# Performance work log

Hardware: AMD Instinct MI355X
Metric: run time of the kernel (lower is better)

## Reference

```python
import jax, jax.numpy as jnp
import numpy as np

N = 50000          # nodes
E = 600000         # edges
D = 128            # g_dim = h1_dim = h2_dim
R = 8              # 2 * n_speakers**2, n_speakers=2
B = 10             # num_bases


def setup_inputs() -> dict:
    key = jax.random.key(0)
    ks = jax.random.split(key, 10)
    s = 1.0 / np.sqrt(D)
    return {
        "node_features": jax.random.normal(ks[0], (N, D), jnp.float32),
        "edge_index": jax.random.randint(ks[1], (2, E), 0, N, jnp.int64),
        "edge_type": jax.random.randint(ks[2], (E,), 0, R, jnp.int64),
        # RGCNConv params (basis decomposition)
        "basis": jax.random.normal(ks[3], (B, D, D), jnp.float32) * s,
        "comp": jax.random.normal(ks[4], (R, B), jnp.float32) * (1.0 / np.sqrt(B)),
        "root": jax.random.normal(ks[5], (D, D), jnp.float32) * s,
        "bias1": jnp.zeros((D,), jnp.float32),
        # GraphConv params
        "w_rel": jax.random.normal(ks[6], (D, D), jnp.float32) * s,
        "b_rel": jnp.zeros((D,), jnp.float32),
        "w_root": jax.random.normal(ks[7], (D, D), jnp.float32) * s,
    }


def reference(node_features, edge_index, edge_type, basis, comp, root, bias1, w_rel, b_rel, w_root):
    x = node_features
    n = x.shape[0]
    r = comp.shape[0]
    src, dst = edge_index[0], edge_index[1]

    # ---- RGCNConv (basis decomposition, per-relation mean aggregation) ----
    # project through bases once: [N, B, D]
    xb = jnp.einsum('ni,bio->nbo', x, basis)
    # per-edge message: combine bases with relation coefficients  [E, D]
    msg = jnp.einsum('eb,ebo->eo', comp[edge_type], xb[src])
    # per-(dst, relation) mean normalization
    seg = dst * r + edge_type                       # [E]
    cnt = jax.ops.segment_sum(jnp.ones((msg.shape[0],), x.dtype), seg, num_segments=n * r)
    norm = 1.0 / jnp.maximum(cnt[seg], 1.0)         # [E]
    agg = jax.ops.segment_sum(msg * norm[:, None], dst, num_segments=n)  # [N, D]
    h1 = agg + x @ root + bias1

    # ---- GraphConv (add aggregation of neighbors + root transform) ----
    nbr = jax.ops.segment_sum(h1[src], dst, num_segments=n)  # [N, D]
    out = nbr @ w_rel.T + b_rel + h1 @ w_root.T
    return out
```

## Files before the change

### kernel.cpp

```cpp
#include <hip/hip_runtime.h>
#include <stdint.h>

#define N_NODES 50000
#define E_EDGES 600000
#define D 128
#define R_REL 8
#define B_BASES 10
#define RN (R_REL * N_NODES)

typedef __attribute__((ext_vector_type(8))) short bf16x8;
typedef __attribute__((ext_vector_type(4))) float f32x4;

__device__ __forceinline__ short f2b(float f) {
    uint32_t u = __float_as_uint(f);
    u += 0x7fff + ((u >> 16) & 1);
    return (short)(u >> 16);
}
__device__ __forceinline__ float b2f(uint16_t u) {
    return __uint_as_float((uint32_t)u << 16);
}

__global__ __launch_bounds__(256) void k_front(const float* __restrict__ x,
                                               unsigned short* __restrict__ xb,
                                               const int* __restrict__ dst,
                                               const int* __restrict__ et,
                                               int* __restrict__ cntr,
                                               const float* __restrict__ basis,
                                               const float* __restrict__ comp,
                                               const float* __restrict__ root,
                                               const float* __restrict__ wrel,
                                               const float* __restrict__ wroot,
                                               short* __restrict__ wt,
                                               short* __restrict__ wrel_b,
                                               short* __restrict__ wroot_b) {
    const int XB_N = N_NODES * D / 8;
    int tid = blockIdx.x * 256 + threadIdx.x;
    if (tid < XB_N) {
        const float4* s = (const float4*)x + (size_t)tid * 2;
        float4 v0 = s[0], v1 = s[1];
        union { uint4 u; unsigned short h[8]; } pk;
        pk.h[0] = (unsigned short)f2b(v0.x); pk.h[1] = (unsigned short)f2b(v0.y);
        pk.h[2] = (unsigned short)f2b(v0.z); pk.h[3] = (unsigned short)f2b(v0.w);
        pk.h[4] = (unsigned short)f2b(v1.x); pk.h[5] = (unsigned short)f2b(v1.y);
        pk.h[6] = (unsigned short)f2b(v1.z); pk.h[7] = (unsigned short)f2b(v1.w);
        ((uint4*)xb)[tid] = pk.u;
    } else if (tid < XB_N + E_EDGES) {
        int e = tid - XB_N;
        atomicAdd(&cntr[dst[e] * R_REL + et[e]], 1);
    } else {
        int t2 = tid - XB_N - E_EDGES;
        if (t2 < 9 * D * D) {
            int s = t2 >> 14;
            int rem = t2 & 16383;
            int j = rem >> 7, i = rem & 127;
            float v;
            if (s < 8) {
                v = 0.f;
#pragma unroll
                for (int b = 0; b < B_BASES; b++)
                    v += comp[s * B_BASES + b] * basis[b * D * D + i * D + j];
            } else {
                v = root[i * D + j];
            }
            wt[t2] = f2b(v);
        } else {
            int t3 = t2 - 9 * D * D;
            if (t3 < D * D) {
                wrel_b[t3]  = f2b(wrel[t3]);
                wroot_b[t3] = f2b(wroot[t3]);
            }
        }
    }
}

__device__ __forceinline__ int wave_scan_incl(int v) {
    int lane = threadIdx.x & 63;
#pragma unroll
    for (int off = 1; off < 64; off <<= 1) {
        int n = __shfl_up(v, off, 64);
        if (lane >= off) v += n;
    }
    return v;
}

__global__ __launch_bounds__(1024) void k_scan_a(const int* __restrict__ in,
                                                 int* __restrict__ out,
                                                 int* __restrict__ bsum, int n) {
    __shared__ int wsum[16];
    int t = threadIdx.x, lane = t & 63, wid = t >> 6;
    int g = blockIdx.x * 1024 + t;
    int v = (g < n) ? in[g] : 0;
    int isc = wave_scan_incl(v);
    if (lane == 63) wsum[wid] = isc;
    __syncthreads();
    if (wid == 0) {
        int wv = (lane < 16) ? wsum[lane] : 0;
        int wsc = wave_scan_incl(wv);
        if (lane < 16) wsum[lane] = wsc - wv;
    }
    __syncthreads();
    if (g < n) out[g] = wsum[wid] + isc - v;
    if (t == 1023 && bsum) bsum[blockIdx.x] = wsum[15] + isc;
}

__global__ __launch_bounds__(1024) void k_scan_c(int* __restrict__ out,
                                                 const int* __restrict__ bsum, int n) {
    int g = blockIdx.x * 1024 + threadIdx.x;
    if (g < n) out[g] += bsum[blockIdx.x];
}

__global__ __launch_bounds__(256) void k_bucket(const int* __restrict__ src,
                                                const int* __restrict__ dst,
                                                const int* __restrict__ et,
                                                int* __restrict__ seg_off,
                                                int* __restrict__ es1) {
    int e = blockIdx.x * 256 + threadIdx.x;
    if (e >= E_EDGES) return;
    int key = dst[e] * R_REL + et[e];
    int pos = atomicAdd(&seg_off[key], 1);
    es1[pos] = src[e];
}

__global__ __launch_bounds__(256) void k_aggmean(const unsigned short* __restrict__ xb,
                                                 const int* __restrict__ es1,
                                                 const int* __restrict__ seg_off,
                                                 unsigned short* __restrict__ mx) {
    int t = threadIdx.x;
    int sw = t >> 4, l = t & 15;
    int k = blockIdx.x * 16 + sw;
    if (k >= RN) return;
    int start = (k == 0) ? 0 : seg_off[k - 1];
    int end = seg_off[k];
    float ax[8];
#pragma unroll
    for (int q = 0; q < 8; q++) ax[q] = 0.f;
    size_t loff = (size_t)l * 8;
    int pos = start;
    for (; pos + 2 <= end; pos += 2) {
        int s0 = es1[pos], s1 = es1[pos + 1];
        uint4 v0 = *(const uint4*)(xb + (size_t)s0 * D + loff);
        uint4 v1 = *(const uint4*)(xb + (size_t)s1 * D + loff);
        const uint32_t* w0 = (const uint32_t*)&v0;
        const uint32_t* w1 = (const uint32_t*)&v1;
#pragma unroll
        for (int q = 0; q < 4; q++) {
            ax[q * 2]     += b2f((uint16_t)w0[q]) + b2f((uint16_t)w1[q]);
            ax[q * 2 + 1] += b2f((uint16_t)(w0[q] >> 16)) + b2f((uint16_t)(w1[q] >> 16));
        }
    }
    if (pos < end) {
        int s0 = es1[pos];
        uint4 v0 = *(const uint4*)(xb + (size_t)s0 * D + loff);
        const uint32_t* w0 = (const uint32_t*)&v0;
#pragma unroll
        for (int q = 0; q < 4; q++) {
            ax[q * 2]     += b2f((uint16_t)w0[q]);
            ax[q * 2 + 1] += b2f((uint16_t)(w0[q] >> 16));
        }
    }
    float nm = (end > start) ? 1.f / (float)(end - start) : 0.f;
    union { uint4 u; unsigned short h[8]; } pk;
#pragma unroll
    for (int q = 0; q < 8; q++) pk.h[q] = (unsigned short)f2b(ax[q] * nm);
    *(uint4*)(mx + (size_t)k * D + loff) = pk.u;
}

__global__ __launch_bounds__(256) void k_h1_gemm(const unsigned short* __restrict__ mx,
                                                 const unsigned short* __restrict__ xb,
                                                 const short* __restrict__ wt,
                                                 const float* __restrict__ bias1,
                                                 unsigned short* __restrict__ h1b) {
    __shared__ short ws[2][128 * 128];
    int t = threadIdx.x;
    int wave = t >> 6, lane = t & 63, quad = lane >> 4, l16 = lane & 15;
    int base = blockIdx.x * 128;
    int n0 = base + wave * 32 + l16;
    int n1 = n0 + 16;
    int nc0 = n0 < N_NODES ? n0 : N_NODES - 1;
    int nc1 = n1 < N_NODES ? n1 : N_NODES - 1;
    int ci0 = wave * 8;

    auto aptr = [&](int nc, int s) -> const unsigned short* {
        return (s < 8) ? mx + ((size_t)nc * 8 + s) * D : xb + (size_t)nc * D;
    };

    uint4 aReg[2][2][4];
    {
        uint4 b0[8];
#pragma unroll
        for (int i = 0; i < 8; i++) {
            int row = (ci0 + i) * 4 + quad;
            b0[i] = *(const uint4*)(wt + row * D + (l16 << 3));
        }
#pragma unroll
        for (int kc = 0; kc < 4; kc++) {
            int co = (kc * 4 + quad) * 8;
            aReg[0][0][kc] = *(const uint4*)(aptr(nc0, 0) + co);
            aReg[0][1][kc] = *(const uint4*)(aptr(nc1, 0) + co);
            aReg[1][0][kc] = *(const uint4*)(aptr(nc0, 1) + co);
            aReg[1][1][kc] = *(const uint4*)(aptr(nc1, 1) + co);
        }
#pragma unroll
        for (int i = 0; i < 8; i++) {
            int row = (ci0 + i) * 4 + quad;
            *(uint4*)&ws[0][row * 128 + ((l16 ^ (row & 15)) << 3)] = b0[i];
        }
    }
    __syncthreads();

    f32x4 acc[2][8];
#pragma unroll
    for (int tl = 0; tl < 2; tl++)
#pragma unroll
        for (int jt = 0; jt < 8; jt++) acc[tl][jt] = (f32x4){0.f, 0.f, 0.f, 0.f};

    for (int s = 0; s < 9; s++) {
        int cur = s & 1;
        uint4 bn[8];
        if (s + 1 < 9) {
            const short* wb = wt + (size_t)(s + 1) * D * D;
#pragma unroll
            for (int i = 0; i < 8; i++) {
                int row = (ci0 + i) * 4 + quad;
                bn[i] = *(const uint4*)(wb + row * D + (l16 << 3));
            }
        }
#pragma unroll
        for (int kc = 0; kc < 4; kc++) {
            int c0 = kc * 4 + quad;
            bf16x8 a0 = *(bf16x8*)&aReg[cur][0][kc];
            bf16x8 a1 = *(bf16x8*)&aReg[cur][1][kc];
#pragma unroll
            for (int jt = 0; jt < 8; jt++) {
                bf16x8 b = *(const bf16x8*)&ws[cur][(jt * 16 + l16) * 128 + ((c0 ^ l16) << 3)];
                acc[0][jt] = __builtin_amdgcn_mfma_f32_16x16x32_bf16(a0, b, acc[0][jt], 0, 0, 0);
                acc[1][jt] = __builtin_amdgcn_mfma_f32_16x16x32_bf16(a1, b, acc[1][jt], 0, 0, 0);
            }
        }
        if (s + 2 <= 8) {
#pragma unroll
            for (int kc = 0; kc < 4; kc++) {
                int co = (kc * 4 + quad) * 8;
                aReg[cur][0][kc] = *(const uint4*)(aptr(nc0, s + 2) + co);
                aReg[cur][1][kc] = *(const uint4*)(aptr(nc1, s + 2) + co);
            }
        }
        if (s + 1 < 9) {
#pragma unroll
            for (int i = 0; i < 8; i++) {
                int row = (ci0 + i) * 4 + quad;
                *(uint4*)&ws[cur ^ 1][row * 128 + ((l16 ^ (row & 15)) << 3)] = bn[i];
            }
        }
        __syncthreads();
    }

#pragma unroll
    for (int tl = 0; tl < 2; tl++) {
#pragma unroll
        for (int reg = 0; reg < 4; reg++) {
            int node = base + wave * 32 + tl * 16 + quad * 4 + reg;
            if (node >= N_NODES) continue;
#pragma unroll
            for (int jt = 0; jt < 8; jt++) {
                int col = jt * 16 + l16;
                float v = acc[tl][jt][reg] + bias1[col];
                h1b[(size_t)node * D + col] = (unsigned short)f2b(v);
            }
        }
    }
}

__global__ __launch_bounds__(256) void k_agg_nbr(const unsigned short* __restrict__ h1b,
                                                 const int* __restrict__ es1,
                                                 const int* __restrict__ seg_off,
                                                 unsigned short* __restrict__ nbr) {
    int t = threadIdx.x;
    int wave = t >> 6, lane = t & 63, sub = lane >> 4, l = lane & 15;
    int d = blockIdx.x * 16 + wave * 4 + sub;
    if (d >= N_NODES) return;
    int start = (d == 0) ? 0 : seg_off[d * R_REL - 1];
    int end = seg_off[d * R_REL + 7];
    float acc[8];
#pragma unroll
    for (int j = 0; j < 8; j++) acc[j] = 0.f;
    size_t loff = (size_t)l * 8;

    int pos = start;
    for (; pos + 4 <= end; pos += 4) {
        int i0 = es1[pos], i1 = es1[pos + 1], i2 = es1[pos + 2], i3 = es1[pos + 3];
        uint4 v0 = *(const uint4*)(h1b + (size_t)i0 * D + loff);
        uint4 v1 = *(const uint4*)(h1b + (size_t)i1 * D + loff);
        uint4 v2 = *(const uint4*)(h1b + (size_t)i2 * D + loff);
        uint4 v3 = *(const uint4*)(h1b + (size_t)i3 * D + loff);
        const uint32_t* w0 = (const uint32_t*)&v0;
        const uint32_t* w1 = (const uint32_t*)&v1;
        const uint32_t* w2 = (const uint32_t*)&v2;
        const uint32_t* w3 = (const uint32_t*)&v3;
#pragma unroll
        for (int q = 0; q < 4; q++) {
            acc[q * 2]     += b2f((uint16_t)w0[q]) + b2f((uint16_t)w1[q]) +
                              b2f((uint16_t)w2[q]) + b2f((uint16_t)w3[q]);
            acc[q * 2 + 1] += b2f((uint16_t)(w0[q] >> 16)) + b2f((uint16_t)(w1[q] >> 16)) +
                              b2f((uint16_t)(w2[q] >> 16)) + b2f((uint16_t)(w3[q] >> 16));
        }
    }
    for (; pos < end; pos++) {
        int i0 = es1[pos];
        uint4 v0 = *(const uint4*)(h1b + (size_t)i0 * D + loff);
        const uint32_t* w0 = (const uint32_t*)&v0;
#pragma unroll
        for (int q = 0; q < 4; q++) {
            acc[q * 2]     += b2f((uint16_t)w0[q]);
            acc[q * 2 + 1] += b2f((uint16_t)(w0[q] >> 16));
        }
    }

    union { uint4 u; unsigned short h[8]; } pk;
#pragma unroll
    for (int j = 0; j < 8; j++) pk.h[j] = (unsigned short)f2b(acc[j]);
    *(uint4*)(nbr + (size_t)d * D + loff) = pk.u;
}

__global__ __launch_bounds__(256) void k_out2(const unsigned short* __restrict__ h1b,
                                              const unsigned short* __restrict__ nbr,
                                              const short* __restrict__ wroot_b,
                                              const short* __restrict__ wrel_b,
                                              const float* __restrict__ brel,
                                              float* __restrict__ out) {
    __shared__ short ws[2][128 * 128];
    int t = threadIdx.x;
    int wave = t >> 6, lane = t & 63, quad = lane >> 4, l16 = lane & 15;
    int base = blockIdx.x * 128;
    int n0 = base + wave * 32 + l16;
    int n1 = n0 + 16;
    int nc0 = n0 < N_NODES ? n0 : N_NODES - 1;
    int nc1 = n1 < N_NODES ? n1 : N_NODES - 1;
    int ci0 = wave * 8;

    uint4 aReg[2][2][4];
    {
        uint4 b0[8];
#pragma unroll
        for (int i = 0; i < 8; i++) {
            int row = (ci0 + i) * 4 + quad;
            b0[i] = *(const uint4*)(wroot_b + row * D + (l16 << 3));
        }
#pragma unroll
        for (int kc = 0; kc < 4; kc++) {
            int co = (kc * 4 + quad) * 8;
            aReg[0][0][kc] = *(const uint4*)(h1b + (size_t)nc0 * D + co);
            aReg[0][1][kc] = *(const uint4*)(h1b + (size_t)nc1 * D + co);
            aReg[1][0][kc] = *(const uint4*)(nbr + (size_t)nc0 * D + co);
            aReg[1][1][kc] = *(const uint4*)(nbr + (size_t)nc1 * D + co);
        }
#pragma unroll
        for (int i = 0; i < 8; i++) {
            int row = (ci0 + i) * 4 + quad;
            *(uint4*)&ws[0][row * 128 + ((l16 ^ (row & 15)) << 3)] = b0[i];
        }
    }
    __syncthreads();

    f32x4 acc[2][8];
#pragma unroll
    for (int tl = 0; tl < 2; tl++)
#pragma unroll
        for (int jt = 0; jt < 8; jt++) acc[tl][jt] = (f32x4){0.f, 0.f, 0.f, 0.f};

#pragma unroll
    for (int s = 0; s < 2; s++) {
        int cur = s & 1;
        uint4 bn[8];
        if (s == 0) {
#pragma unroll
            for (int i = 0; i < 8; i++) {
                int row = (ci0 + i) * 4 + quad;
                bn[i] = *(const uint4*)(wrel_b + row * D + (l16 << 3));
            }
        }
#pragma unroll
        for (int kc = 0; kc < 4; kc++) {
            int c0 = kc * 4 + quad;
            bf16x8 a0 = *(bf16x8*)&aReg[cur][0][kc];
            bf16x8 a1 = *(bf16x8*)&aReg[cur][1][kc];
#pragma unroll
            for (int jt = 0; jt < 8; jt++) {
                bf16x8 b = *(const bf16x8*)&ws[cur][(jt * 16 + l16) * 128 + ((c0 ^ l16) << 3)];
                acc[0][jt] = __builtin_amdgcn_mfma_f32_16x16x32_bf16(a0, b, acc[0][jt], 0, 0, 0);
                acc[1][jt] = __builtin_amdgcn_mfma_f32_16x16x32_bf16(a1, b, acc[1][jt], 0, 0, 0);
            }
        }
        if (s == 0) {
#pragma unroll
            for (int i = 0; i < 8; i++) {
                int row = (ci0 + i) * 4 + quad;
                *(uint4*)&ws[1][row * 128 + ((l16 ^ (row & 15)) << 3)] = bn[i];
            }
            __syncthreads();
        }
    }

#pragma unroll
    for (int tl = 0; tl < 2; tl++) {
#pragma unroll
        for (int reg = 0; reg < 4; reg++) {
            int node = base + wave * 32 + tl * 16 + quad * 4 + reg;
            if (node >= N_NODES) continue;
#pragma unroll
            for (int jt = 0; jt < 8; jt++) {
                int col = jt * 16 + l16;
                out[(size_t)node * D + col] = acc[tl][jt][reg] + brel[col];
            }
        }
    }
}

extern "C" void kernel_launch(void* const* d_in, const int* in_sizes, int n_in,
                              void* d_out, int out_size, void* d_ws, size_t ws_size,
                              hipStream_t stream) {
    const float* x     = (const float*)d_in[0];
    const int*   ei    = (const int*)d_in[1];
    const int*   et    = (const int*)d_in[2];
    const float* basis = (const float*)d_in[3];
    const float* comp  = (const float*)d_in[4];
    const float* root  = (const float*)d_in[5];
    const float* bias1 = (const float*)d_in[6];
    const float* wrel  = (const float*)d_in[7];
    const float* brel  = (const float*)d_in[8];
    const float* wroot = (const float*)d_in[9];
    float* out = (float*)d_out;
    const int* src = ei;
    const int* dst = ei + E_EDGES;

    char* p = (char*)d_ws;
    auto alloc = [&](size_t bytes) { char* q = p; p += (bytes + 255) & ~(size_t)255; return q; };
    short* wt      = (short*)alloc((size_t)9 * D * D * sizeof(short));
    short* wrel_b  = (short*)alloc(D * D * sizeof(short));
    short* wroot_b = (short*)alloc(D * D * sizeof(short));
    int*   cntr    = (int*)alloc((size_t)RN * sizeof(int));
    int*   seg_off = (int*)alloc((size_t)RN * sizeof(int));
    int*   es1     = (int*)alloc((size_t)(E_EDGES + 16) * sizeof(int));
    int*   bsum    = (int*)alloc(1024 * sizeof(int));
    unsigned short* xb  = (unsigned short*)alloc((size_t)N_NODES * D * sizeof(unsigned short));
    unsigned short* mx  = (unsigned short*)alloc((size_t)RN * D * sizeof(unsigned short));
    unsigned short* h1b = (unsigned short*)alloc((size_t)N_NODES * D * sizeof(unsigned short));
    unsigned short* nbr = xb;

    hipMemsetAsync(cntr, 0, (size_t)RN * sizeof(int), stream);

    const int XB_N = N_NODES * D / 8;
    int nfront = (XB_N + E_EDGES + 9 * D * D + D * D + 255) / 256;
    k_front<<<nfront, 256, 0, stream>>>(x, xb, dst, et, cntr,
                                        basis, comp, root, wrel, wroot,
                                        wt, wrel_b, wroot_b);

    int nscan = (RN + 1023) / 1024;
    k_scan_a<<<nscan, 1024, 0, stream>>>(cntr, seg_off, bsum, RN);
    k_scan_a<<<1, 1024, 0, stream>>>(bsum, bsum, nullptr, nscan);
    k_scan_c<<<nscan, 1024, 0, stream>>>(seg_off, bsum, RN);

    k_bucket<<<(E_EDGES + 255) / 256, 256, 0, stream>>>(src, dst, et, seg_off, es1);

    k_aggmean<<<RN / 16, 256, 0, stream>>>(xb, es1, seg_off, mx);

    int nb2 = (N_NODES + 127) / 128;
    int na = (N_NODES + 15) / 16;
    k_h1_gemm<<<nb2, 256, 0, stream>>>(mx, xb, wt, bias1, h1b);
    k_agg_nbr<<<na, 256, 0, stream>>>(h1b, es1, seg_off, nbr);
    k_out2<<<nb2, 256, 0, stream>>>(h1b, nbr, wroot_b, wrel_b, brel, out);
}
```

Baseline: 265.2 us.

## Shrink h1 GEMM tile, single-buffer LDS, relation-major mean layout

Switches the mean-aggregation output to a relation-major layout [R][N][D], with xb stored as the ninth slab, so the h1 GEMM reads contiguous per-relation planes. The GEMM tile shrinks from 128 to 64 nodes per block and uses a single 32KB LDS weight buffer with an extra barrier, plus launch bounds set to 3 blocks. The goal is higher occupancy and more blocks for latency hiding. The cost is twice as many weight reloads per node and more synchronisation per step.

```diff
diff --git a/kernel.cpp b/kernel.cpp
--- a/kernel.cpp
+++ b/kernel.cpp
@@ -162,111 +162,97 @@
     union { uint4 u; unsigned short h[8]; } pk;
 #pragma unroll
     for (int q = 0; q < 8; q++) pk.h[q] = (unsigned short)f2b(ax[q] * nm);
-    *(uint4*)(mx + (size_t)k * D + loff) = pk.u;
-}
-
-__global__ __launch_bounds__(256) void k_h1_gemm(const unsigned short* __restrict__ mx,
-                                                 const unsigned short* __restrict__ xb,
-                                                 const short* __restrict__ wt,
-                                                 const float* __restrict__ bias1,
-                                                 unsigned short* __restrict__ h1b) {
-    __shared__ short ws[2][128 * 128];
+    size_t krow = (size_t)(k & 7) * N_NODES + (size_t)(k >> 3);
+    *(uint4*)(mx + krow * D + loff) = pk.u;
+}
+
+__global__ __launch_bounds__(256, 3) void k_h1_gemm(const unsigned short* __restrict__ mxall,
+                                                    const short* __restrict__ wt,
+                                                    const float* __restrict__ bias1,
+                                                    unsigned short* __restrict__ h1b) {
+    __shared__ short ws[128 * 128];
     int t = threadIdx.x;
     int wave = t >> 6, lane = t & 63, quad = lane >> 4, l16 = lane & 15;
-    int base = blockIdx.x * 128;
-    int n0 = base + wave * 32 + l16;
-    int n1 = n0 + 16;
+    int base = blockIdx.x * 64;
+    int n0 = base + wave * 16 + l16;
     int nc0 = n0 < N_NODES ? n0 : N_NODES - 1;
-    int nc1 = n1 < N_NODES ? n1 : N_NODES - 1;
     int ci0 = wave * 8;
 
-    auto aptr = [&](int nc, int s) -> const unsigned short* {
-        return (s < 8) ? mx + ((size_t)nc * 8 + s) * D : xb + (size_t)nc * D;
-    };
-
-    uint4 aReg[2][2][4];
-    {
-        uint4 b0[8];
-#pragma unroll
-        for (int i = 0; i < 8; i++) {
-            int row = (ci0 + i) * 4 + quad;
-            b0[i] = *(const uint4*)(wt + row * D + (l16 << 3));
-        }
-#pragma unroll
-        for (int kc = 0; kc < 4; kc++) {
-            int co = (kc * 4 + quad) * 8;
-            aReg[0][0][kc] = *(const uint4*)(aptr(nc0, 0) + co);
-            aReg[0][1][kc] = *(const uint4*)(aptr(nc1, 0) + co);
-            aReg[1][0][kc] = *(const uint4*)(aptr(nc0, 1) + co);
-            aReg[1][1][kc] = *(const uint4*)(aptr(nc1, 1) + co);
-        }
-#pragma unroll
-        for (int i = 0; i < 8; i++) {
-            int row = (ci0 + i) * 4 + quad;
-            *(uint4*)&ws[0][row * 128 + ((l16 ^ (row & 15)) << 3)] = b0[i];
-        }
+    uint4 aReg[2][4];
+    uint4 wn[8];
+
+#pragma unroll
+    for (int i = 0; i < 8; i++) {
+        int row = (ci0 + i) * 4 + quad;
+        wn[i] = *(const uint4*)(wt + row * D + (l16 << 3));
+    }
+#pragma unroll
+    for (int kc = 0; kc < 4; kc++) {
+        int co = (kc * 4 + quad) * 8;
+        aReg[0][kc] = *(const uint4*)(mxall + ((size_t)0 * N_NODES + nc0) * D + co);
+        aReg[1][kc] = *(const uint4*)(mxall + ((size_t)1 * N_NODES + nc0) * D + co);
+    }
+#pragma unroll
+    for (int i = 0; i < 8; i++) {
+        int row = (ci0 + i) * 4 + quad;
+        *(uint4*)&ws[row * 128 + ((l16 ^ (row & 15)) << 3)] = wn[i];
     }
     __syncthreads();
 
-    f32x4 acc[2][8];
-#pragma unroll
-    for (int tl = 0; tl < 2; tl++)
-#pragma unroll
-        for (int jt = 0; jt < 8; jt++) acc[tl][jt] = (f32x4){0.f, 0.f, 0.f, 0.f};
-
+    f32x4 acc[8];
+#pragma unroll
+    for (int jt = 0; jt < 8; jt++) acc[jt] = (f32x4){0.f, 0.f, 0.f, 0.f};
+
+#pragma unroll
     for (int s = 0; s < 9; s++) {
-        int cur = s & 1;
-        uint4 bn[8];
+        const int par = s & 1;
+        bf16x8 a[4];
+#pragma unroll
+        for (int kc = 0; kc < 4; kc++) a[kc] = *(bf16x8*)&aReg[par][kc];
+        if (s + 2 < 9) {
+#pragma unroll
+            for (int kc = 0; kc < 4; kc++) {
+                int co = (kc * 4 + quad) * 8;
+                aReg[par][kc] = *(const uint4*)(mxall + ((size_t)(s + 2) * N_NODES + nc0) * D + co);
+            }
+        }
         if (s + 1 < 9) {
             const short* wb = wt + (size_t)(s + 1) * D * D;
 #pragma unroll
             for (int i = 0; i < 8; i++) {
                 int row = (ci0 + i) * 4 + quad;
-                bn[i] = *(const uint4*)(wb + row * D + (l16 << 3));
+                wn[i] = *(const uint4*)(wb + row * D + (l16 << 3));
             }
         }
 #pragma unroll
         for (int kc = 0; kc < 4; kc++) {
             int c0 = kc * 4 + quad;
-            bf16x8 a0 = *(bf16x8*)&aReg[cur][0][kc];
-            bf16x8 a1 = *(bf16x8*)&aReg[cur][1][kc];
 #pragma unroll
             for (int jt = 0; jt < 8; jt++) {
-                bf16x8 b = *(const bf16x8*)&ws[cur][(jt * 16 + l16) * 128 + ((c0 ^ l16) << 3)];
-                acc[0][jt] = __builtin_amdgcn_mfma_f32_16x16x32_bf16(a0, b, acc[0][jt], 0, 0, 0);
-                acc[1][jt] = __builtin_amdgcn_mfma_f32_16x16x32_bf16(a1, b, acc[1][jt], 0, 0, 0);
-            }
-        }
-        if (s + 2 <= 8) {
-#pragma unroll
-            for (int kc = 0; kc < 4; kc++) {
-                int co = (kc * 4 + quad) * 8;
-                aReg[cur][0][kc] = *(const uint4*)(aptr(nc0, s + 2) + co);
-                aReg[cur][1][kc] = *(const uint4*)(aptr(nc1, s + 2) + co);
+                bf16x8 b = *(const bf16x8*)&ws[(jt * 16 + l16) * 128 + ((c0 ^ l16) << 3)];
+                acc[jt] = __builtin_amdgcn_mfma_f32_16x16x32_bf16(a[kc], b, acc[jt], 0, 0, 0);
             }
         }
         if (s + 1 < 9) {
+            __syncthreads();
 #pragma unroll
             for (int i = 0; i < 8; i++) {
                 int row = (ci0 + i) * 4 + quad;
-                *(uint4*)&ws[cur ^ 1][row * 128 + ((l16 ^ (row & 15)) << 3)] = bn[i];
-            }
-        }
-        __syncthreads();
-    }
-
-#pragma unroll
-    for (int tl = 0; tl < 2; tl++) {
-#pragma unroll
-        for (int reg = 0; reg < 4; reg++) {
-            int node = base + wave * 32 + tl * 16 + quad * 4 + reg;
-            if (node >= N_NODES) continue;
-#pragma unroll
-            for (int jt = 0; jt < 8; jt++) {
-                int col = jt * 16 + l16;
-                float v = acc[tl][jt][reg] + bias1[col];
-                h1b[(size_t)node * D + col] = (unsigned short)f2b(v);
-            }
+                *(uint4*)&ws[row * 128 + ((l16 ^ (row & 15)) << 3)] = wn[i];
+            }
+            __syncthreads();
+        }
+    }
+
+#pragma unroll
+    for (int reg = 0; reg < 4; reg++) {
+        int node = base + wave * 16 + quad * 4 + reg;
+        if (node >= N_NODES) continue;
+#pragma unroll
+        for (int jt = 0; jt < 8; jt++) {
+            int col = jt * 16 + l16;
+            float v = acc[jt][reg] + bias1[col];
+            h1b[(size_t)node * D + col] = (unsigned short)f2b(v);
         }
     }
 }
@@ -442,10 +428,11 @@
     int*   seg_off = (int*)alloc((size_t)RN * sizeof(int));
     int*   es1     = (int*)alloc((size_t)(E_EDGES + 16) * sizeof(int));
     int*   bsum    = (int*)alloc(1024 * sizeof(int));
-    unsigned short* xb  = (unsigned short*)alloc((size_t)N_NODES * D * sizeof(unsigned short));
-    unsigned short* mx  = (unsigned short*)alloc((size_t)RN * D * sizeof(unsigned short));
-    unsigned short* h1b = (unsigned short*)alloc((size_t)N_NODES * D * sizeof(unsigned short));
-    unsigned short* nbr = xb;
+    unsigned short* mxall = (unsigned short*)alloc((size_t)9 * N_NODES * D * sizeof(unsigned short));
+    unsigned short* h1b   = (unsigned short*)alloc((size_t)N_NODES * D * sizeof(unsigned short));
+    unsigned short* xb  = mxall + (size_t)8 * N_NODES * D;
+    unsigned short* mx  = mxall;
+    unsigned short* nbr = mxall;
 
     hipMemsetAsync(cntr, 0, (size_t)RN * sizeof(int), stream);
 
@@ -464,9 +451,10 @@
 
     k_aggmean<<<RN / 16, 256, 0, stream>>>(xb, es1, seg_off, mx);
 
+    int nbh = (N_NODES + 63) / 64;
     int nb2 = (N_NODES + 127) / 128;
     int na = (N_NODES + 15) / 16;
-    k_h1_gemm<<<nb2, 256, 0, stream>>>(mx, xb, wt, bias1, h1b);
+    k_h1_gemm<<<nbh, 256, 0, stream>>>(mxall, wt, bias1, h1b);
     k_agg_nbr<<<na, 256, 0, stream>>>(h1b, es1, seg_off, nbr);
     k_out2<<<nb2, 256, 0, stream>>>(h1b, nbr, wroot_b, wrel_b, brel, out);
 }
```

New measurement: 328.4 us. 1.24x slower.
